# Kernel optimization log

Measured on AMD Instinct MI355X. Metric: run time of the kernel, lower is better.

Reference implementation:

```python
import itertools
import jax, jax.numpy as jnp
import numpy as np

N = 1024


def _static(n):
    # Static (trace-time) index/mask structures, identical to the torch module.
    rail_shape = (2, 2, n + 1, n + 1)
    im = np.zeros(rail_shape, dtype=bool)
    im[0, :, 1:, 1:] = True
    im[1, :, :-1, :-1] = True
    om = np.zeros(rail_shape, dtype=bool)
    om[0, :, :-1, :-1] = True
    om[1, :, 1:, 1:] = True
    # 8 bit patterns over the 3 leave-one-out inputs -> (8, 3)
    bits = np.asarray(list(itertools.product(range(2), repeat=3)), dtype=np.float32)
    in_idx = np.nonzero(im.reshape(-1))[0]   # 4*n*n gather indices
    out_idx = np.nonzero(om.reshape(-1))[0]  # 4*n*n scatter indices
    return in_idx, out_idx, bits


def setup_inputs() -> dict:
    key = jax.random.key(0)
    k1, k2, k3 = jax.random.split(key, 3)
    n = N
    rail_len = 4 * (n + 1) ** 2
    return {
        "x": jax.random.uniform(k1, (n,), jnp.float32),
        "toggle_gates": jax.random.normal(k2, (4, 8, n, n), jnp.float32),
        "rail_state": jax.random.uniform(k3, (rail_len,), jnp.float32),
        "mask": jnp.ones((rail_len,), jnp.int32),
    }


def reference(x, toggle_gates, rail_state, mask):
    n = toggle_gates.shape[-1]
    in_idx, out_idx, bits = _static(n)

    # Write input x into rail_state[1, 1, :len(x), 0] (view write in torch).
    rail = rail_state.reshape(2, 2, n + 1, n + 1)
    rail = rail.at[1, 1, : x.shape[0], 0].set(x).reshape(-1)

    # Gather the 4 input planes: (4, n, n)
    new_inputs = rail[in_idx].reshape(4, n, n)
    tw = jax.nn.sigmoid(toggle_gates)  # (4, 8, n, n)

    bits_b = jnp.asarray(bits)[:, :, None, None]  # (8, 3, 1, 1)
    others = np.array([[j for j in range(4) if j != i] for i in range(4)])

    outs = []
    for i in range(4):  # fixed small loop over the 4 rail directions
        inp_i = new_inputs[others[i]]  # (3, n, n) leave-one-out inputs
        # soft AND over bit patterns: (8, n, n)
        w = jnp.prod(1.0 - jnp.abs(bits_b - inp_i[None]), axis=1)
        toggled = tw[i] * new_inputs[i] + (1.0 - tw[i]) * (1.0 - new_inputs[i])
        outs.append((toggled * w).sum(0))  # (n, n)

    new_out = jnp.clip(jnp.stack(outs).reshape(-1), 0.0, 1.0)
    rail = rail.at[out_idx].set(new_out)

    # mask is all-ones, so rail[mask] == rail; multiply keeps shape static.
    return rail * mask.astype(rail.dtype) * toggle_gates.reshape(-1)[0]
```

## Files before the change

kernel.cpp:

```cpp
#include <hip/hip_runtime.h>


constexpr int N     = 1024;
constexpr int NP1   = N + 1;
constexpr int PLANE = NP1 * NP1;
constexpr int NN    = N * N;

__device__ __forceinline__ float sigmoidf_fast(float t) {
    return __builtin_amdgcn_rcpf(1.0f + __expf(-t));
}

__global__ __launch_bounds__(256) void asic_main(
    const float* __restrict__ x,
    const float* __restrict__ tg,
    const float* __restrict__ rail,
    const int*  __restrict__ mask,
    float* __restrict__ out)
{
    const int tid  = blockIdx.x * 256 + threadIdx.x;
    const int pix0 = tid << 2;
    const int r    = pix0 >> 10;
    const int c0   = pix0 & (N - 1);
    const float g0 = tg[0];

    float u[4][4];
    const int b01 = (r + 1) * NP1 + (c0 + 1);
    const int b23 = r * NP1 + c0;
#pragma unroll
    for (int q = 0; q < 4; ++q) {
        u[0][q] = rail[0 * PLANE + b01 + q];
        u[1][q] = rail[1 * PLANE + b01 + q];
        u[2][q] = rail[2 * PLANE + b23 + q];
        u[3][q] = rail[3 * PLANE + b23 + q];
    }
    if (c0 == 0) u[3][0] = x[r];

    float F0[4][4], F1[4][4];
#pragma unroll
    for (int j = 0; j < 4; ++j)
#pragma unroll
        for (int q = 0; q < 4; ++q) {
            F0[j][q] = 1.0f - fabsf(u[j][q]);
            F1[j][q] = 1.0f - fabsf(1.0f - u[j][q]);
        }

#pragma unroll
    for (int i = 0; i < 4; ++i) {
        const int o0 = (i == 0) ? 1 : 0;
        const int o1 = (i <= 1) ? 2 : 1;
        const int o2 = (i <= 2) ? 3 : 2;

        float h00[4], h01[4], h10[4], h11[4];
#pragma unroll
        for (int q = 0; q < 4; ++q) {
            h00[q] = F0[o1][q] * F0[o2][q];
            h01[q] = F0[o1][q] * F1[o2][q];
            h10[q] = F1[o1][q] * F0[o2][q];
            h11[q] = F1[o1][q] * F1[o2][q];
        }

        float s0[4] = {0.f, 0.f, 0.f, 0.f};
        float s1[4] = {0.f, 0.f, 0.f, 0.f};
#pragma unroll
        for (int p = 0; p < 8; ++p) {
            const float4 tv =
                *reinterpret_cast<const float4*>(&tg[(i * 8 + p) * NN + pix0]);
            const float tw[4] = { sigmoidf_fast(tv.x), sigmoidf_fast(tv.y),
                                  sigmoidf_fast(tv.z), sigmoidf_fast(tv.w) };
            const int b0 = p >> 2, b1 = (p >> 1) & 1, b2 = p & 1;
#pragma unroll
            for (int q = 0; q < 4; ++q) {
                const float fa = b0 ? F1[o0][q] : F0[o0][q];
                const float hb = b1 ? (b2 ? h11[q] : h10[q])
                                    : (b2 ? h01[q] : h00[q]);
                const float w  = fa * hb;
                s0[q] += w;
                s1[q]  = fmaf(tw[q], w, s1[q]);
            }
        }

#pragma unroll
        for (int q = 0; q < 4; ++q) {
            const float A = 2.0f * u[i][q] - 1.0f;
            const float B = 1.0f - u[i][q];
            float acc = fmaf(A, s1[q], B * s0[q]);
            acc = fminf(fmaxf(acc, 0.0f), 1.0f);
            const int flat = (i < 2) ? (i * PLANE + r * NP1 + (c0 + q))
                                     : (i * PLANE + (r + 1) * NP1 + (c0 + q + 1));
            out[flat] = acc * (float)mask[flat] * g0;
        }
    }
}

__global__ __launch_bounds__(256) void asic_boundary(
    const float* __restrict__ x,
    const float* __restrict__ tg,
    const float* __restrict__ rail,
    const int*  __restrict__ mask,
    float* __restrict__ out)
{
    const int per = 2 * N + 1;
    const int idx = blockIdx.x * 256 + threadIdx.x;
    if (idx >= 4 * per) return;
    const int plane = idx / per;
    const int k = idx % per;

    int r, c;
    if (plane < 2) {
        if (k <= N) { r = N; c = k; }
        else        { r = k - (N + 1); c = N; }
    } else {
        if (k <= N) { r = 0; c = k; }
        else        { r = k - N; c = 0; }
    }

    const int flat = plane * PLANE + r * NP1 + c;
    float v;
    if (plane == 3 && c == 0 && r < N) v = x[r];
    else                               v = rail[flat];
    out[flat] = v * (float)mask[flat] * tg[0];
}

extern "C" void kernel_launch(void* const* d_in, const int* in_sizes, int n_in,
                              void* d_out, int out_size, void* d_ws, size_t ws_size,
                              hipStream_t stream) {
    const float* x    = (const float*)d_in[0];
    const float* tg   = (const float*)d_in[1];
    const float* rail = (const float*)d_in[2];
    const int*   mask = (const int*)d_in[3];
    float* out = (float*)d_out;

    asic_main<<<(NN / 4) / 256, 256, 0, stream>>>(x, tg, rail, mask, out);

    const int nb = 4 * (2 * N + 1);
    asic_boundary<<<(nb + 255) / 256, 256, 0, stream>>>(x, tg, rail, mask, out);
}
```

Baseline: 229.7 us.

## Fuse boundary kernel into main kernel and use nontemporal loads/stores

Folds the boundary-copy work into the first threads of the main kernel so only one launch is needed. The 128MB toggle-gate stream is read with nontemporal loads and outputs are written with nontemporal stores to reduce cache pollution. Per-direction factor terms are recomputed instead of precomputing pairwise products, and launch bounds request 5 blocks per CU to limit register use. The recomputation adds some ALU work and the occupancy hint may force register spilling.

```diff
diff --git a/kernel.cpp b/kernel.cpp
--- a/kernel.cpp
+++ b/kernel.cpp
@@ -6,11 +6,13 @@
 constexpr int PLANE = NP1 * NP1;
 constexpr int NN    = N * N;
 
+typedef float floatx4 __attribute__((ext_vector_type(4)));
+
 __device__ __forceinline__ float sigmoidf_fast(float t) {
     return __builtin_amdgcn_rcpf(1.0f + __expf(-t));
 }
 
-__global__ __launch_bounds__(256) void asic_main(
+__global__ __launch_bounds__(256, 5) void asic_fused(
     const float* __restrict__ x,
     const float* __restrict__ tg,
     const float* __restrict__ rail,
@@ -18,10 +20,30 @@
     float* __restrict__ out)
 {
     const int tid  = blockIdx.x * 256 + threadIdx.x;
+    const float g0 = tg[0];
+
+    {
+        const int per = 2 * N + 1;
+        if (tid < 4 * per) {
+            const int plane = tid / per;
+            const int k = tid % per;
+            int r, c;
+            if (plane < 2) {
+                if (k <= N) { r = N; c = k; }
+                else        { r = k - (N + 1); c = N; }
+            } else {
+                if (k <= N) { r = 0; c = k; }
+                else        { r = k - N; c = 0; }
+            }
+            const int flat = plane * PLANE + r * NP1 + c;
+            float v = (plane == 3 && c == 0 && r < N) ? x[r] : rail[flat];
+            out[flat] = v * (float)mask[flat] * g0;
+        }
+    }
+
     const int pix0 = tid << 2;
     const int r    = pix0 >> 10;
     const int c0   = pix0 & (N - 1);
-    const float g0 = tg[0];
 
     float u[4][4];
     const int b01 = (r + 1) * NP1 + (c0 + 1);
@@ -35,45 +57,34 @@
     }
     if (c0 == 0) u[3][0] = x[r];
 
-    float F0[4][4], F1[4][4];
-#pragma unroll
-    for (int j = 0; j < 4; ++j)
-#pragma unroll
-        for (int q = 0; q < 4; ++q) {
-            F0[j][q] = 1.0f - fabsf(u[j][q]);
-            F1[j][q] = 1.0f - fabsf(1.0f - u[j][q]);
-        }
-
 #pragma unroll
     for (int i = 0; i < 4; ++i) {
         const int o0 = (i == 0) ? 1 : 0;
         const int o1 = (i <= 1) ? 2 : 1;
         const int o2 = (i <= 2) ? 3 : 2;
 
-        float h00[4], h01[4], h10[4], h11[4];
+        float A0[4], A1[4], B0[4], B1[4], C0[4], C1[4];
 #pragma unroll
         for (int q = 0; q < 4; ++q) {
-            h00[q] = F0[o1][q] * F0[o2][q];
-            h01[q] = F0[o1][q] * F1[o2][q];
-            h10[q] = F1[o1][q] * F0[o2][q];
-            h11[q] = F1[o1][q] * F1[o2][q];
+            A0[q] = 1.0f - fabsf(u[o0][q]);  A1[q] = 1.0f - fabsf(1.0f - u[o0][q]);
+            B0[q] = 1.0f - fabsf(u[o1][q]);  B1[q] = 1.0f - fabsf(1.0f - u[o1][q]);
+            C0[q] = 1.0f - fabsf(u[o2][q]);  C1[q] = 1.0f - fabsf(1.0f - u[o2][q]);
         }
 
         float s0[4] = {0.f, 0.f, 0.f, 0.f};
         float s1[4] = {0.f, 0.f, 0.f, 0.f};
 #pragma unroll
         for (int p = 0; p < 8; ++p) {
-            const float4 tv =
-                *reinterpret_cast<const float4*>(&tg[(i * 8 + p) * NN + pix0]);
+            const floatx4 tv = __builtin_nontemporal_load(
+                reinterpret_cast<const floatx4*>(&tg[(i * 8 + p) * NN + pix0]));
             const float tw[4] = { sigmoidf_fast(tv.x), sigmoidf_fast(tv.y),
                                   sigmoidf_fast(tv.z), sigmoidf_fast(tv.w) };
             const int b0 = p >> 2, b1 = (p >> 1) & 1, b2 = p & 1;
 #pragma unroll
             for (int q = 0; q < 4; ++q) {
-                const float fa = b0 ? F1[o0][q] : F0[o0][q];
-                const float hb = b1 ? (b2 ? h11[q] : h10[q])
-                                    : (b2 ? h01[q] : h00[q]);
-                const float w  = fa * hb;
+                const float w = (b0 ? A1[q] : A0[q]) *
+                                (b1 ? B1[q] : B0[q]) *
+                                (b2 ? C1[q] : C0[q]);
                 s0[q] += w;
                 s1[q]  = fmaf(tw[q], w, s1[q]);
             }
@@ -87,38 +98,9 @@
             acc = fminf(fmaxf(acc, 0.0f), 1.0f);
             const int flat = (i < 2) ? (i * PLANE + r * NP1 + (c0 + q))
                                      : (i * PLANE + (r + 1) * NP1 + (c0 + q + 1));
-            out[flat] = acc * (float)mask[flat] * g0;
+            __builtin_nontemporal_store(acc * (float)mask[flat] * g0, &out[flat]);
         }
     }
-}
-
-__global__ __launch_bounds__(256) void asic_boundary(
-    const float* __restrict__ x,
-    const float* __restrict__ tg,
-    const float* __restrict__ rail,
-    const int*  __restrict__ mask,
-    float* __restrict__ out)
-{
-    const int per = 2 * N + 1;
-    const int idx = blockIdx.x * 256 + threadIdx.x;
-    if (idx >= 4 * per) return;
-    const int plane = idx / per;
-    const int k = idx % per;
-
-    int r, c;
-    if (plane < 2) {
-        if (k <= N) { r = N; c = k; }
-        else        { r = k - (N + 1); c = N; }
-    } else {
-        if (k <= N) { r = 0; c = k; }
-        else        { r = k - N; c = 0; }
-    }
-
-    const int flat = plane * PLANE + r * NP1 + c;
-    float v;
-    if (plane == 3 && c == 0 && r < N) v = x[r];
-    else                               v = rail[flat];
-    out[flat] = v * (float)mask[flat] * tg[0];
 }
 
 extern "C" void kernel_launch(void* const* d_in, const int* in_sizes, int n_in,
@@ -130,8 +112,5 @@
     const int*   mask = (const int*)d_in[3];
     float* out = (float*)d_out;
 
-    asic_main<<<(NN / 4) / 256, 256, 0, stream>>>(x, tg, rail, mask, out);
-
-    const int nb = 4 * (2 * N + 1);
-    asic_boundary<<<(nb + 255) / 256, 256, 0, stream>>>(x, tg, rail, mask, out);
+    asic_fused<<<(NN / 4) / 256, 256, 0, stream>>>(x, tg, rail, mask, out);
 }
```

New measurement: 225.2 us. 2.0% less time.
